# Kernel optimization log

Hardware: AMD Instinct MI355X
Metric: run time of the kernel (lower is better)

Reference implementation:

```python
import jax, jax.numpy as jnp
import numpy as np

STRIDE = (1, 1)
PADDING = ((1, 1), (1, 1))  # symmetric padding of 1 on H and W
DILATION = (1, 1)


def setup_inputs() -> dict:
    key = jax.random.key(0)
    k1, k2 = jax.random.split(key)
    x = jax.random.normal(k1, (32, 128, 56, 56), dtype=jnp.float32)
    weight = jax.random.normal(k2, (256, 128, 3, 3), dtype=jnp.float32) * 0.05
    return {"x": x, "weight": weight}


def reference(x, weight):
    # Faithful math of the im2col + matmul conv: identical to a standard
    # cross-correlation Conv2d with stride=1, padding=1, dilation=1, groups=1,
    # bias=False. Expressed as a single fused conv instead of the python-loop
    # gather + stacked GEMM of the original (same output values).
    out = jax.lax.conv_general_dilated(
        x, weight,
        window_strides=STRIDE,
        padding=PADDING,
        rhs_dilation=DILATION,
        dimension_numbers=("NCHW", "OIHW", "NCHW"),
        feature_group_count=1,
    )
    return out  # [B, C_out, H_out, W_out] = [32, 256, 56, 56]
```

## Files before the change

### kernel.cpp

```cpp
#include <hip/hip_runtime.h>
#include <stdint.h>


#define CIN   128
#define HW_   56
#define CO_   256
#define KSZ   1152
#define IMGHW 3136
#define HP    58
#define NT    18
#define BUFSZ 65536
#define XT_BYTES ((size_t)32 * HP * HP * CIN * 2)
#define WP_BYTES ((size_t)CO_ * KSZ * 2)
#define WS_NEED  (XT_BYTES + WP_BYTES)

typedef __attribute__((ext_vector_type(8))) __bf16 bf16x8;
typedef __attribute__((ext_vector_type(4))) float f32x4;
typedef __attribute__((ext_vector_type(8))) unsigned short ushort8;

__device__ __forceinline__ unsigned short f2bf(float f) {
    unsigned int u = __float_as_uint(f);
    u += 0x7fffu + ((u >> 16) & 1u);
    return (unsigned short)(u >> 16);
}

__device__ __forceinline__ void gl2lds16(const void* g, void* l) {
    __builtin_amdgcn_global_load_lds(
        (const __attribute__((address_space(1))) void*)g,
        (__attribute__((address_space(3))) void*)l, 16, 0, 0);
}

__global__ void pack_weight(const float* __restrict__ w,
                            unsigned short* __restrict__ wp) {
    int idx = blockIdx.x * 256 + threadIdx.x;
    int co = idx / KSZ;
    int k  = idx - co * KSZ;
    int khkw = k >> 7;
    int ci = k & 127;
    wp[idx] = f2bf(w[(co * CIN + ci) * 9 + khkw]);
}

__global__ __launch_bounds__(256)
void xform(const float* __restrict__ x, unsigned short* __restrict__ xt) {
    const int nb = blockIdx.x;
    const int n  = nb / HP;
    const int hp = nb - n * HP;
    unsigned short* orow = xt + ((size_t)n * HP + hp) * (HP * CIN);
    const int t = threadIdx.x;

    if (hp == 0 || hp == HP - 1) {
        for (int i = t; i < (HP * CIN) / 8; i += 256)
            ((ushort8*)orow)[i] = (ushort8){0, 0, 0, 0, 0, 0, 0, 0};
        return;
    }
    const int h = hp - 1;
    __shared__ unsigned short T[CIN][HP];
    const int wl = t & 63, cg = t >> 6;
    for (int c0 = 0; c0 < CIN; c0 += 4) {
        int ci = c0 + cg;
        if (wl < HW_)
            T[ci][wl] = f2bf(x[(((size_t)n * CIN + ci) * HW_ + h) * HW_ + wl]);
    }
    __syncthreads();
    const int ci = t & 127, wo = t >> 7;
    for (int wp_ = wo; wp_ < HP; wp_ += 2) {
        unsigned short v = 0;
        if (wp_ >= 1 && wp_ <= HW_) v = T[ci][wp_ - 1];
        orow[wp_ * CIN + ci] = v;
    }
}

__global__ __launch_bounds__(512, 2)
void conv2p(const unsigned short* __restrict__ xt,
            const unsigned short* __restrict__ wpk,
            float* __restrict__ out)
{
    __shared__ __align__(16) char lds[2 * BUFSZ];

    const int tid  = threadIdx.x;
    const int lane = tid & 63;
    const int wid  = tid >> 6;

    int bid = blockIdx.x;
    bid = (bid & 7) * 49 + (bid >> 3);
    const int m0 = bid << 8;

    const int lc = (tid & 3) ^ ((tid >> 2) & 3) ^ ((tid >> 4) & 3);
    uint32_t aoff[2], boff[2];
    #pragma unroll
    for (int p = 0; p < 2; ++p) {
        int m = m0 + (tid >> 2) + p * 128;
        int n = m / IMGHW;
        int rem = m - n * IMGHW;
        int h = rem / HW_;
        int w = rem - h * HW_;
        aoff[p] = (uint32_t)((((n * HP + h) * HP + w) << 8) + (lc << 4));
        boff[p] = (uint32_t)(((tid >> 2) + p * 128) * (KSZ * 2) + (lc << 4));
    }

    const int fr = lane & 15, fg = lane >> 4;
    const int sw = (fr & 3) ^ ((fr >> 2) & 3);
    const int cswz = (fg ^ sw) << 4;
    const int wm0 = (wid >> 2) << 7;
    const int wn0 = (wid & 3) << 6;
    const int aRB = (wm0 + fr) * 64 + cswz;
    const int bRB = 32768 + (wn0 + fr) * 64 + cswz;

    const char* xtc = (const char*)xt;
    const char* wpc = (const char*)wpk;

    f32x4 acc[8][4];
    #pragma unroll
    for (int i = 0; i < 8; ++i)
        #pragma unroll
        for (int j = 0; j < 4; ++j)
            acc[i][j] = (f32x4){0.f, 0.f, 0.f, 0.f};

    auto STAGE = [&](int t, int kh) {
        const int bufo = (t & 1) * BUFSZ;
        int tap = t >> 1;
        int khr = (tap * 11) >> 5;
        int kwr = tap - khr * 3;
        uint32_t asl = (uint32_t)(((khr * HP + kwr) << 8) + ((t & 1) << 7) + (kh << 6));
        uint32_t bsl = (uint32_t)((t << 7) + (kh << 6));
        char* DA = &lds[bufo + kh * 16384];
        char* DB = &lds[bufo + 32768 + kh * 16384];
        gl2lds16(xtc + aoff[0] + asl, DA + tid * 16);
        gl2lds16(xtc + aoff[1] + asl, DA + 8192 + tid * 16);
        gl2lds16(wpc + boff[0] + bsl, DB + tid * 16);
        gl2lds16(wpc + boff[1] + bsl, DB + 8192 + tid * 16);
    };

    auto PHASE = [&](int t, int kh) {
        const char* L = lds + (t & 1) * BUFSZ + kh * 16384;
        ushort8 breg[4], areg[8];
        #pragma unroll
        for (int nf = 0; nf < 4; ++nf)
            breg[nf] = *(const ushort8*)(L + bRB + nf * 1024);
        #pragma unroll
        for (int mf = 0; mf < 8; ++mf)
            areg[mf] = *(const ushort8*)(L + aRB + mf * 1024);

        if (t + 1 < NT) STAGE(t + 1, kh);

        if (t + 1 < NT)      asm volatile("s_waitcnt vmcnt(4)" ::: "memory");
        else if (kh == 0)    asm volatile("s_waitcnt vmcnt(0)" ::: "memory");
        __builtin_amdgcn_sched_barrier(0);
        __builtin_amdgcn_s_barrier();

        __builtin_amdgcn_s_setprio(1);
        #pragma unroll
        for (int mf = 0; mf < 8; ++mf)
            #pragma unroll
            for (int nf = 0; nf < 4; ++nf)
                acc[mf][nf] = __builtin_amdgcn_mfma_f32_16x16x32_bf16(
                    __builtin_bit_cast(bf16x8, breg[nf]),
                    __builtin_bit_cast(bf16x8, areg[mf]),
                    acc[mf][nf], 0, 0, 0);
        __builtin_amdgcn_s_setprio(0);
    };

    STAGE(0, 0); STAGE(0, 1);
    asm volatile("s_waitcnt vmcnt(4)" ::: "memory");
    __builtin_amdgcn_s_barrier();

    #pragma unroll 1
    for (int t = 0; t < NT; ++t) {
        PHASE(t, 0);
        PHASE(t, 1);
    }

    const int mwave = m0 + wm0;
    const int co0 = wn0 + (fg << 2);
    #pragma unroll
    for (int mf = 0; mf < 8; ++mf) {
        int m = mwave + mf * 16 + fr;
        int n = m / IMGHW;
        int hwr = m - n * IMGHW;
        uint32_t basem = (uint32_t)(n * (CO_ * IMGHW) + hwr);
        #pragma unroll
        for (int nf = 0; nf < 4; ++nf)
            #pragma unroll
            for (int q = 0; q < 4; ++q)
                out[basem + (uint32_t)(co0 + nf * 16 + q) * IMGHW] = acc[mf][nf][q];
    }
}

#define BM    64
#define BK    32
#define NSTEP 36
#define LDSP  40

template<bool PACKED>
__global__ __launch_bounds__(256, 2)
void conv_fb(const float* __restrict__ x,
             const float* __restrict__ wraw,
             const unsigned short* __restrict__ wp,
             float* __restrict__ out)
{
    __shared__ __align__(16) unsigned short Al[2][BM][LDSP];
    __shared__ __align__(16) unsigned short Bl[2][CO_][LDSP];

    const int tid  = threadIdx.x;
    const int lane = tid & 63;
    const int wid  = tid >> 6;

    const int mb    = blockIdx.x;
    const int n_img = mb / 49;
    const int hw0   = (mb - n_img * 49) * BM;

    const int mm = lane;
    const int hw = hw0 + mm;
    const int h  = hw / HW_;
    const int w_ = hw - h * HW_;

    const int bco  = tid >> 2;
    const int bkkg = tid & 3;

    float   aPF[8];
    ushort8 bPF[4];

    auto loadA = [&](int step) {
        int khkw = step >> 2;
        int kh = khkw / 3, kw = khkw - (khkw / 3) * 3;
        int ci0 = (step & 3) * BK + wid * 8;
        int ih = h + kh - 1, iw = w_ + kw - 1;
        bool valid = ((unsigned)ih < (unsigned)HW_) && ((unsigned)iw < (unsigned)HW_);
        const float* px = x + (((size_t)(n_img * CIN + ci0) * HW_ + ih) * HW_ + iw);
        #pragma unroll
        for (int e = 0; e < 8; ++e)
            aPF[e] = valid ? px[e * IMGHW] : 0.f;
    };
    auto writeA = [&](int buf) {
        ushort8 v;
        #pragma unroll
        for (int e = 0; e < 8; ++e) v[e] = f2bf(aPF[e]);
        *(ushort8*)&Al[buf][mm][wid * 8] = v;
    };
    auto loadB = [&](int step) {
        if (PACKED) {
            int k0 = step * BK;
            #pragma unroll
            for (int r = 0; r < 4; ++r)
                bPF[r] = *(const ushort8*)&wp[(r * 64 + bco) * KSZ + k0 + bkkg * 8];
        } else {
            int khkw = step >> 2;
            int ci0 = (step & 3) * BK + bkkg * 8;
            #pragma unroll
            for (int r = 0; r < 4; ++r) {
                int co = r * 64 + bco;
                ushort8 v;
                #pragma unroll
                for (int e = 0; e < 8; ++e)
                    v[e] = f2bf(wraw[(co * CIN + ci0 + e) * 9 + khkw]);
                bPF[r] = v;
            }
        }
    };
    auto writeB = [&](int buf) {
        #pragma unroll
        for (int r = 0; r < 4; ++r)
            *(ushort8*)&Bl[buf][r * 64 + bco][bkkg * 8] = bPF[r];
    };

    f32x4 acc[4][4];
    #pragma unroll
    for (int i = 0; i < 4; ++i)
        #pragma unroll
        for (int j = 0; j < 4; ++j)
            acc[i][j] = (f32x4){0.f, 0.f, 0.f, 0.f};

    const int frow = lane & 15;
    const int fk   = (lane >> 4) * 8;

    loadA(0); loadB(0);
    writeA(0); writeB(0);
    __syncthreads();

    for (int s = 0; s < NSTEP; ++s) {
        const int cur = s & 1;
        if (s + 1 < NSTEP) { loadA(s + 1); loadB(s + 1); }

        ushort8 aF[4], bF[4];
        #pragma unroll
        for (int i = 0; i < 4; ++i)
            aF[i] = *(const ushort8*)&Bl[cur][wid * 64 + i * 16 + frow][fk];
        #pragma unroll
        for (int j = 0; j < 4; ++j)
            bF[j] = *(const ushort8*)&Al[cur][j * 16 + frow][fk];

        #pragma unroll
        for (int i = 0; i < 4; ++i)
            #pragma unroll
            for (int j = 0; j < 4; ++j)
                acc[i][j] = __builtin_amdgcn_mfma_f32_16x16x32_bf16(
                    __builtin_bit_cast(bf16x8, aF[i]),
                    __builtin_bit_cast(bf16x8, bF[j]),
                    acc[i][j], 0, 0, 0);

        if (s + 1 < NSTEP) { writeA(cur ^ 1); writeB(cur ^ 1); }
        __syncthreads();
    }

    float* ob = out + (size_t)n_img * (CO_ * IMGHW) + hw0;
    #pragma unroll
    for (int i = 0; i < 4; ++i) {
        int co0 = wid * 64 + i * 16 + (lane >> 4) * 4;
        #pragma unroll
        for (int j = 0; j < 4; ++j) {
            int mcol = j * 16 + (lane & 15);
            #pragma unroll
            for (int q = 0; q < 4; ++q)
                ob[(size_t)(co0 + q) * IMGHW + mcol] = acc[i][j][q];
        }
    }
}

extern "C" void kernel_launch(void* const* d_in, const int* in_sizes, int n_in,
                              void* d_out, int out_size, void* d_ws, size_t ws_size,
                              hipStream_t stream) {
    (void)in_sizes; (void)n_in; (void)out_size;
    const float* x  = (const float*)d_in[0];
    const float* wt = (const float*)d_in[1];
    float* out = (float*)d_out;

    if (ws_size >= WS_NEED) {
        unsigned short* xt  = (unsigned short*)d_ws;
        unsigned short* wpk = (unsigned short*)((char*)d_ws + XT_BYTES);
        xform<<<32 * HP, 256, 0, stream>>>(x, xt);
        pack_weight<<<(CO_ * KSZ) / 256, 256, 0, stream>>>(wt, wpk);
        conv2p<<<392, 512, 0, stream>>>(xt, wpk, out);
    } else if (ws_size >= WP_BYTES) {
        unsigned short* wpk = (unsigned short*)d_ws;
        pack_weight<<<(CO_ * KSZ) / 256, 256, 0, stream>>>(wt, wpk);
        conv_fb<true><<<100352 / BM, 256, 0, stream>>>(x, wt, wpk, out);
    } else {
        conv_fb<false><<<100352 / BM, 256, 0, stream>>>(x, wt, nullptr, out);
    }
}
```

Baseline: 100.5 us.

## Double-buffer LDS fragment registers and change LDS swizzle layout in conv kernel

```diff
diff --git a/kernel.cpp b/kernel.cpp
--- a/kernel.cpp
+++ b/kernel.cpp
@@ -71,7 +71,7 @@
 }
 
 __global__ __launch_bounds__(512, 2)
-void conv2p(const unsigned short* __restrict__ xt,
+void convrd(const unsigned short* __restrict__ xt,
             const unsigned short* __restrict__ wpk,
             float* __restrict__ out)
 {
@@ -85,26 +85,26 @@
     bid = (bid & 7) * 49 + (bid >> 3);
     const int m0 = bid << 8;
 
-    const int lc = (tid & 3) ^ ((tid >> 2) & 3) ^ ((tid >> 4) & 3);
+    const int lc = (tid & 7) ^ ((tid >> 3) & 7);
     uint32_t aoff[2], boff[2];
     #pragma unroll
     for (int p = 0; p < 2; ++p) {
-        int m = m0 + (tid >> 2) + p * 128;
+        int r = p * 128 + ((tid >> 3) << 1) + (lc >> 2);
+        int m = m0 + r;
         int n = m / IMGHW;
         int rem = m - n * IMGHW;
         int h = rem / HW_;
         int w = rem - h * HW_;
-        aoff[p] = (uint32_t)((((n * HP + h) * HP + w) << 8) + (lc << 4));
-        boff[p] = (uint32_t)(((tid >> 2) + p * 128) * (KSZ * 2) + (lc << 4));
+        aoff[p] = (uint32_t)((((n * HP + h) * HP + w) << 8) + ((lc & 3) << 4));
+        boff[p] = (uint32_t)(r * (KSZ * 2) + ((lc & 3) << 4));
     }
 
     const int fr = lane & 15, fg = lane >> 4;
-    const int sw = (fr & 3) ^ ((fr >> 2) & 3);
-    const int cswz = (fg ^ sw) << 4;
+    const int cp = (((fr & 1) << 2) | fg) ^ ((fr >> 1) & 7);
     const int wm0 = (wid >> 2) << 7;
     const int wn0 = (wid & 3) << 6;
-    const int aRB = (wm0 + fr) * 64 + cswz;
-    const int bRB = 32768 + (wn0 + fr) * 64 + cswz;
+    const int aRB = (((wm0 >> 1) + (fr >> 1)) << 7) + (cp << 4);
+    const int bRB = (((wn0 >> 1) + (fr >> 1)) << 7) + (cp << 4);
 
     const char* xtc = (const char*)xt;
     const char* wpc = (const char*)wpk;
@@ -115,6 +115,9 @@
         #pragma unroll
         for (int j = 0; j < 4; ++j)
             acc[i][j] = (f32x4){0.f, 0.f, 0.f, 0.f};
+
+    ushort8 a0[8], b0[4];
+    ushort8 a1[8], b1[4];
 
     auto STAGE = [&](int t, int kh) {
         const int bufo = (t & 1) * BUFSZ;
@@ -131,43 +134,56 @@
         gl2lds16(wpc + boff[1] + bsl, DB + 8192 + tid * 16);
     };
 
-    auto PHASE = [&](int t, int kh) {
-        const char* L = lds + (t & 1) * BUFSZ + kh * 16384;
-        ushort8 breg[4], areg[8];
-        #pragma unroll
-        for (int nf = 0; nf < 4; ++nf)
-            breg[nf] = *(const ushort8*)(L + bRB + nf * 1024);
-        #pragma unroll
-        for (int mf = 0; mf < 8; ++mf)
-            areg[mf] = *(const ushort8*)(L + aRB + mf * 1024);
-
-        if (t + 1 < NT) STAGE(t + 1, kh);
-
-        if (t + 1 < NT)      asm volatile("s_waitcnt vmcnt(4)" ::: "memory");
-        else if (kh == 0)    asm volatile("s_waitcnt vmcnt(0)" ::: "memory");
-        __builtin_amdgcn_sched_barrier(0);
-        __builtin_amdgcn_s_barrier();
-
-        __builtin_amdgcn_s_setprio(1);
-        #pragma unroll
-        for (int mf = 0; mf < 8; ++mf)
-            #pragma unroll
-            for (int nf = 0; nf < 4; ++nf)
-                acc[mf][nf] = __builtin_amdgcn_mfma_f32_16x16x32_bf16(
-                    __builtin_bit_cast(bf16x8, breg[nf]),
-                    __builtin_bit_cast(bf16x8, areg[mf]),
-                    acc[mf][nf], 0, 0, 0);
-        __builtin_amdgcn_s_setprio(0);
-    };
-
-    STAGE(0, 0); STAGE(0, 1);
+    #define LOADF(A_, B_, Apl, Bpl) do { \
+        _Pragma("unroll") for (int i_ = 0; i_ < 4; ++i_) \
+            B_[i_] = *(const ushort8*)((Bpl) + bRB + i_ * 1024); \
+        _Pragma("unroll") for (int i_ = 0; i_ < 8; ++i_) \
+            A_[i_] = *(const ushort8*)((Apl) + aRB + i_ * 1024); \
+    } while (0)
+
+    #define MMALL(A_, B_) do { \
+        _Pragma("unroll") for (int mf_ = 0; mf_ < 8; ++mf_) \
+            _Pragma("unroll") for (int nf_ = 0; nf_ < 4; ++nf_) \
+                acc[mf_][nf_] = __builtin_amdgcn_mfma_f32_16x16x32_bf16( \
+                    __builtin_bit_cast(bf16x8, B_[nf_]), \
+                    __builtin_bit_cast(bf16x8, A_[mf_]), \
+                    acc[mf_][nf_], 0, 0, 0); \
+    } while (0)
+
+    STAGE(0, 0); STAGE(0, 1); STAGE(1, 0);
     asm volatile("s_waitcnt vmcnt(4)" ::: "memory");
     __builtin_amdgcn_s_barrier();
+    LOADF(a0, b0, lds + 0, lds + 32768);
 
     #pragma unroll 1
     for (int t = 0; t < NT; ++t) {
-        PHASE(t, 0);
-        PHASE(t, 1);
+        const int bufo = (t & 1) * BUFSZ;
+        const char* L  = lds + bufo;
+        const char* Ln = lds + (bufo ^ BUFSZ);
+
+        LOADF(a1, b1, L + 16384, L + 49152);
+        if (t + 1 < NT) STAGE(t + 1, 1);
+        __builtin_amdgcn_sched_barrier(0);
+        __builtin_amdgcn_s_setprio(1);
+        MMALL(a0, b0);
+        __builtin_amdgcn_s_setprio(0);
+        __builtin_amdgcn_sched_barrier(0);
+        if (t + 1 < NT)
+            asm volatile("s_waitcnt vmcnt(4)" ::: "memory");
+        __builtin_amdgcn_s_barrier();
+
+        if (t + 1 < NT) LOADF(a0, b0, Ln + 0, Ln + 32768);
+        if (t + 2 < NT) STAGE(t + 2, 0);
+        __builtin_amdgcn_sched_barrier(0);
+        __builtin_amdgcn_s_setprio(1);
+        MMALL(a1, b1);
+        __builtin_amdgcn_s_setprio(0);
+        __builtin_amdgcn_sched_barrier(0);
+        if (t + 2 < NT)
+            asm volatile("s_waitcnt vmcnt(4)" ::: "memory");
+        else if (t + 1 < NT)
+            asm volatile("s_waitcnt vmcnt(0)" ::: "memory");
+        __builtin_amdgcn_s_barrier();
     }
 
     const int mwave = m0 + wm0;
@@ -184,6 +200,8 @@
             for (int q = 0; q < 4; ++q)
                 out[basem + (uint32_t)(co0 + nf * 16 + q) * IMGHW] = acc[mf][nf][q];
     }
+    #undef LOADF
+    #undef MMALL
 }
 
 #define BM    64
@@ -329,7 +347,7 @@
         unsigned short* wpk = (unsigned short*)((char*)d_ws + XT_BYTES);
         xform<<<32 * HP, 256, 0, stream>>>(x, xt);
         pack_weight<<<(CO_ * KSZ) / 256, 256, 0, stream>>>(wt, wpk);
-        conv2p<<<392, 512, 0, stream>>>(xt, wpk, out);
+        convrd<<<392, 512, 0, stream>>>(xt, wpk, out);
     } else if (ws_size >= WP_BYTES) {
         unsigned short* wpk = (unsigned short*)d_ws;
         pack_weight<<<(CO_ * KSZ) / 256, 256, 0, stream>>>(wt, wpk);
```

After: 99.97 us. Within noise of the previous version (-0.5%).

## Restructure conv LDS layout into 128B rows with four-subphase staged prefetch

Applied to the files above, without the earlier changes.

```diff
diff --git a/kernel.cpp b/kernel.cpp
--- a/kernel.cpp
+++ b/kernel.cpp
@@ -54,24 +54,36 @@
         return;
     }
     const int h = hp - 1;
-    __shared__ unsigned short T[CIN][HP];
-    const int wl = t & 63, cg = t >> 6;
-    for (int c0 = 0; c0 < CIN; c0 += 4) {
-        int ci = c0 + cg;
-        if (wl < HW_)
-            T[ci][wl] = f2bf(x[(((size_t)n * CIN + ci) * HW_ + h) * HW_ + wl]);
+    __shared__ ushort2 T[CIN][31];
+    {
+        const int ci = t >> 1, part = t & 1;
+        const float* src = x + (((size_t)n * CIN + ci) * IMGHW + h * HW_ + part * 28);
+        #pragma unroll
+        for (int j = 0; j < 7; ++j) {
+            float4 v = *(const float4*)(src + 4 * j);
+            T[ci][part * 14 + 2 * j]     = (ushort2){f2bf(v.x), f2bf(v.y)};
+            T[ci][part * 14 + 2 * j + 1] = (ushort2){f2bf(v.z), f2bf(v.w)};
+        }
     }
     __syncthreads();
-    const int ci = t & 127, wo = t >> 7;
-    for (int wp_ = wo; wp_ < HP; wp_ += 2) {
-        unsigned short v = 0;
-        if (wp_ >= 1 && wp_ <= HW_) v = T[ci][wp_ - 1];
-        orow[wp_ * CIN + ci] = v;
+    const int wpg = t >> 4, cig = t & 15;
+    const int ci0 = cig * 8;
+    for (int wp_ = wpg; wp_ < HP; wp_ += 16) {
+        ushort8 v = (ushort8){0, 0, 0, 0, 0, 0, 0, 0};
+        const int w_ = wp_ - 1;
+        if ((unsigned)w_ < (unsigned)HW_) {
+            #pragma unroll
+            for (int e = 0; e < 8; ++e) {
+                ushort2 p = T[ci0 + e][w_ >> 1];
+                v[e] = (w_ & 1) ? p.y : p.x;
+            }
+        }
+        *(ushort8*)(orow + wp_ * CIN + ci0) = v;
     }
 }
 
 __global__ __launch_bounds__(512, 2)
-void conv2p(const unsigned short* __restrict__ xt,
+void conv1b(const unsigned short* __restrict__ xt,
             const unsigned short* __restrict__ wpk,
             float* __restrict__ out)
 {
@@ -85,26 +97,28 @@
     bid = (bid & 7) * 49 + (bid >> 3);
     const int m0 = bid << 8;
 
-    const int lc = (tid & 3) ^ ((tid >> 2) & 3) ^ ((tid >> 4) & 3);
-    uint32_t aoff[2], boff[2];
+    const int lc = (tid & 7) ^ ((tid >> 3) & 7);
+    uint32_t aoff[4], boff[4];
     #pragma unroll
-    for (int p = 0; p < 2; ++p) {
-        int m = m0 + (tid >> 2) + p * 128;
+    for (int q = 0; q < 4; ++q) {
+        int m = m0 + q * 64 + (tid >> 3);
         int n = m / IMGHW;
         int rem = m - n * IMGHW;
         int h = rem / HW_;
         int w = rem - h * HW_;
-        aoff[p] = (uint32_t)((((n * HP + h) * HP + w) << 8) + (lc << 4));
-        boff[p] = (uint32_t)(((tid >> 2) + p * 128) * (KSZ * 2) + (lc << 4));
+        aoff[q] = (uint32_t)((((n * HP + h) * HP + w) << 8) + (lc << 4));
+        boff[q] = (uint32_t)((q * 64 + (tid >> 3)) * (KSZ * 2) + (lc << 4));
     }
 
     const int fr = lane & 15, fg = lane >> 4;
-    const int sw = (fr & 3) ^ ((fr >> 2) & 3);
-    const int cswz = (fg ^ sw) << 4;
+    const int cK0 = ((fg ^ (fr & 7)) << 4);
+    const int cK1 = (((4 | fg) ^ (fr & 7)) << 4);
     const int wm0 = (wid >> 2) << 7;
     const int wn0 = (wid & 3) << 6;
-    const int aRB = (wm0 + fr) * 64 + cswz;
-    const int bRB = 32768 + (wn0 + fr) * 64 + cswz;
+    const int APB = (wid >> 2) ? 16384 : 0;
+    const int BPB = 32768 + ((wid & 2) ? 16384 : 0);
+    const int aBase = APB + fr * 128;
+    const int bBase = BPB + ((wid & 1) * 64 + fr) * 128;
 
     const char* xtc = (const char*)xt;
     const char* wpc = (const char*)wpk;
@@ -116,58 +130,112 @@
         for (int j = 0; j < 4; ++j)
             acc[i][j] = (f32x4){0.f, 0.f, 0.f, 0.f};
 
-    auto STAGE = [&](int t, int kh) {
-        const int bufo = (t & 1) * BUFSZ;
-        int tap = t >> 1;
+    ushort8 areg[4], breg[4];
+
+    auto STAGE = [&](int tt, int sp) {
+        const int bo = (tt & 1) << 16;
+        int tap = tt >> 1;
         int khr = (tap * 11) >> 5;
         int kwr = tap - khr * 3;
-        uint32_t asl = (uint32_t)(((khr * HP + kwr) << 8) + ((t & 1) << 7) + (kh << 6));
-        uint32_t bsl = (uint32_t)((t << 7) + (kh << 6));
-        char* DA = &lds[bufo + kh * 16384];
-        char* DB = &lds[bufo + 32768 + kh * 16384];
-        gl2lds16(xtc + aoff[0] + asl, DA + tid * 16);
-        gl2lds16(xtc + aoff[1] + asl, DA + 8192 + tid * 16);
-        gl2lds16(wpc + boff[0] + bsl, DB + tid * 16);
-        gl2lds16(wpc + boff[1] + bsl, DB + 8192 + tid * 16);
+        uint32_t asl = (uint32_t)(((khr * HP + kwr) << 8) + ((tt & 1) << 7));
+        uint32_t bsl = (uint32_t)(tt << 7);
+        char* L = &lds[bo];
+        switch (sp) {
+        case 0:
+            gl2lds16(xtc + aoff[0] + asl, L + 0     + tid * 16);
+            gl2lds16(xtc + aoff[2] + asl, L + 16384 + tid * 16);
+            break;
+        case 1:
+            gl2lds16(wpc + boff[0] + bsl, L + 32768 + tid * 16);
+            gl2lds16(wpc + boff[1] + bsl, L + 40960 + tid * 16);
+            break;
+        case 2:
+            gl2lds16(wpc + boff[2] + bsl, L + 49152 + tid * 16);
+            gl2lds16(wpc + boff[3] + bsl, L + 57344 + tid * 16);
+            break;
+        default:
+            gl2lds16(xtc + aoff[1] + asl, L + 8192  + tid * 16);
+            gl2lds16(xtc + aoff[3] + asl, L + 24576 + tid * 16);
+            break;
+        }
     };
 
-    auto PHASE = [&](int t, int kh) {
-        const char* L = lds + (t & 1) * BUFSZ + kh * 16384;
-        ushort8 breg[4], areg[8];
-        #pragma unroll
-        for (int nf = 0; nf < 4; ++nf)
-            breg[nf] = *(const ushort8*)(L + bRB + nf * 1024);
-        #pragma unroll
-        for (int mf = 0; mf < 8; ++mf)
-            areg[mf] = *(const ushort8*)(L + aRB + mf * 1024);
-
-        if (t + 1 < NT) STAGE(t + 1, kh);
-
-        if (t + 1 < NT)      asm volatile("s_waitcnt vmcnt(4)" ::: "memory");
-        else if (kh == 0)    asm volatile("s_waitcnt vmcnt(0)" ::: "memory");
-        __builtin_amdgcn_sched_barrier(0);
-        __builtin_amdgcn_s_barrier();
-
-        __builtin_amdgcn_s_setprio(1);
-        #pragma unroll
-        for (int mf = 0; mf < 8; ++mf)
-            #pragma unroll
-            for (int nf = 0; nf < 4; ++nf)
-                acc[mf][nf] = __builtin_amdgcn_mfma_f32_16x16x32_bf16(
-                    __builtin_bit_cast(bf16x8, breg[nf]),
-                    __builtin_bit_cast(bf16x8, areg[mf]),
-                    acc[mf][nf], 0, 0, 0);
-        __builtin_amdgcn_s_setprio(0);
-    };
-
-    STAGE(0, 0); STAGE(0, 1);
-    asm volatile("s_waitcnt vmcnt(4)" ::: "memory");
+    #define SBAR0 __builtin_amdgcn_sched_barrier(0)
+    #define MM16(mbase) do { \
+        _Pragma("unroll") for (int mf_ = 0; mf_ < 4; ++mf_) \
+            _Pragma("unroll") for (int nf_ = 0; nf_ < 4; ++nf_) \
+                acc[(mbase) + mf_][nf_] = __builtin_amdgcn_mfma_f32_16x16x32_bf16( \
+                    __builtin_bit_cast(bf16x8, breg[nf_]), \
+                    __builtin_bit_cast(bf16x8, areg[mf_]), \
+                    acc[(mbase) + mf_][nf_], 0, 0, 0); \
+    } while (0)
+
+    STAGE(0, 0); STAGE(0, 1); STAGE(0, 2); STAGE(0, 3);
+    asm volatile("s_waitcnt vmcnt(2)" ::: "memory");
     __builtin_amdgcn_s_barrier();
 
     #pragma unroll 1
     for (int t = 0; t < NT; ++t) {
-        PHASE(t, 0);
-        PHASE(t, 1);
+        const int bo = (t & 1) << 16;
+        const char* L = lds + bo;
+        const bool pf = (t + 1 < NT);
+
+        #pragma unroll
+        for (int nf = 0; nf < 4; ++nf)
+            breg[nf] = *(const ushort8*)(L + bBase + nf * 2048 + cK0);
+        #pragma unroll
+        for (int mf = 0; mf < 4; ++mf)
+            areg[mf] = *(const ushort8*)(L + aBase + mf * 2048 + cK0);
+        if (pf) STAGE(t + 1, 0);
+        SBAR0;
+        if (pf) asm volatile("s_waitcnt vmcnt(2)" ::: "memory");
+        else    asm volatile("s_waitcnt vmcnt(0)" ::: "memory");
+        __builtin_amdgcn_s_barrier();
+        asm volatile("s_waitcnt lgkmcnt(0)" ::: "memory");
+        SBAR0;
+        __builtin_amdgcn_s_setprio(1);
+        MM16(0);
+        __builtin_amdgcn_s_setprio(0);
+
+        #pragma unroll
+        for (int mf = 0; mf < 4; ++mf)
+            areg[mf] = *(const ushort8*)(L + aBase + (mf + 4) * 2048 + cK0);
+        if (pf) STAGE(t + 1, 1);
+        SBAR0;
+        __builtin_amdgcn_s_barrier();
+        asm volatile("s_waitcnt lgkmcnt(0)" ::: "memory");
+        SBAR0;
+        __builtin_amdgcn_s_setprio(1);
+        MM16(4);
+        __builtin_amdgcn_s_setprio(0);
+
+        #pragma unroll
+        for (int nf = 0; nf < 4; ++nf)
+            breg[nf] = *(const ushort8*)(L + bBase + nf * 2048 + cK1);
+        #pragma unroll
+        for (int mf = 0; mf < 4; ++mf)
+            areg[mf] = *(const ushort8*)(L + aBase + mf * 2048 + cK1);
+        if (pf) STAGE(t + 1, 2);
+        SBAR0;
+        __builtin_amdgcn_s_barrier();
+        asm volatile("s_waitcnt lgkmcnt(0)" ::: "memory");
+        SBAR0;
+        __builtin_amdgcn_s_setprio(1);
+        MM16(0);
+        __builtin_amdgcn_s_setprio(0);
+
+        #pragma unroll
+        for (int mf = 0; mf < 4; ++mf)
+            areg[mf] = *(const ushort8*)(L + aBase + (mf + 4) * 2048 + cK1);
+        if (pf) STAGE(t + 1, 3);
+        SBAR0;
+        if (pf) asm volatile("s_waitcnt vmcnt(2)" ::: "memory");
+        __builtin_amdgcn_s_barrier();
+        asm volatile("s_waitcnt lgkmcnt(0)" ::: "memory");
+        SBAR0;
+        __builtin_amdgcn_s_setprio(1);
+        MM16(4);
+        __builtin_amdgcn_s_setprio(0);
     }
 
     const int mwave = m0 + wm0;
@@ -184,6 +252,8 @@
             for (int q = 0; q < 4; ++q)
                 out[basem + (uint32_t)(co0 + nf * 16 + q) * IMGHW] = acc[mf][nf][q];
     }
+    #undef SBAR0
+    #undef MM16
 }
 
 #define BM    64
@@ -329,7 +399,7 @@
         unsigned short* wpk = (unsigned short*)((char*)d_ws + XT_BYTES);
         xform<<<32 * HP, 256, 0, stream>>>(x, xt);
         pack_weight<<<(CO_ * KSZ) / 256, 256, 0, stream>>>(wt, wpk);
-        conv2p<<<392, 512, 0, stream>>>(xt, wpk, out);
+        conv1b<<<392, 512, 0, stream>>>(xt, wpk, out);
     } else if (ws_size >= WP_BYTES) {
         unsigned short* wpk = (unsigned short*)d_ws;
         pack_weight<<<(CO_ * KSZ) / 256, 256, 0, stream>>>(wt, wpk);
```

Result: faster. 93.49 us (-6.9%).
